# Optimization experiments

Hardware: AMD Instinct MI355X
Metric: run time of the kernel (lower is better)

## Reference

```python
import jax, jax.numpy as jnp
import numpy as np

B, S, D = 4, 2048, 2048
H = 16
DH = D // H  # 128

def _rope_tables(seq_len, d_head, base=10000.0):
    inv_freq = 1.0 / (base ** (np.arange(0, d_head, 2, dtype=np.float32) / d_head))
    pos = np.arange(seq_len, dtype=np.float32)
    ang = pos[:, None] * inv_freq[None, :]  # (S, d_head/2)
    return jnp.asarray(np.cos(ang)), jnp.asarray(np.sin(ang))

def setup_inputs() -> dict:
    key = jax.random.key(0)
    ks = jax.random.split(key, 4)
    x = jax.random.normal(ks[0], (B, S, D), dtype=jnp.float32)
    rope_cos, rope_sin = _rope_tables(S, DH)
    # Linear params, scaled like torch default init (~1/sqrt(fan_in))
    Wqkv = jax.random.normal(ks[1], (D, 3 * D), dtype=jnp.float32) / np.sqrt(D)
    bqkv = jnp.zeros((3 * D,), dtype=jnp.float32)
    Wout = jax.random.normal(ks[2], (D, D), dtype=jnp.float32) / np.sqrt(D)
    bout = jnp.zeros((D,), dtype=jnp.float32)
    return {"x": x, "rope_cos": rope_cos, "rope_sin": rope_sin,
            "Wqkv": Wqkv, "bqkv": bqkv, "Wout": Wout, "bout": bout}

def _apply_rope(x, cos, sin):
    # x: (B, H, S, DH); cos/sin: (S, DH/2), broadcast over B,H
    x1 = x[..., 0::2]
    x2 = x[..., 1::2]
    out = jnp.stack([x1 * cos - x2 * sin, x1 * sin + x2 * cos], axis=-1)
    return out.reshape(*out.shape[:-2], -1)  # interleave back to (..., DH)

def reference(x, rope_cos, rope_sin, Wqkv, bqkv, Wout, bout):
    qkv = (x @ Wqkv + bqkv).reshape(B, S, 3, H, DH)
    qkv = jnp.transpose(qkv, (2, 0, 3, 1, 4))  # (3, B, H, S, DH)
    q, k, v = qkv[0], qkv[1], qkv[2]
    q = _apply_rope(q, rope_cos, rope_sin)
    k = _apply_rope(k, rope_cos, rope_sin)
    scale = 1.0 / np.sqrt(DH)
    scores = jnp.einsum('bhqd,bhkd->bhqk', q, k) * scale  # (B,H,S,S)
    causal = jnp.tril(jnp.ones((S, S), dtype=bool))
    scores = jnp.where(causal, scores, jnp.finfo(scores.dtype).min)
    attn = jax.nn.softmax(scores, axis=-1)
    out = jnp.einsum('bhqk,bhkd->bhqd', attn, v)  # (B,H,S,DH)
    out = jnp.transpose(out, (0, 2, 1, 3)).reshape(B, S, D)
    return out @ Wout + bout
```

## Files before the change

kernel.cpp:

```cpp
#include <hip/hip_runtime.h>
#include <hip/hip_bf16.h>
#include <math.h>

typedef __attribute__((ext_vector_type(8))) short bf16x8;
typedef __attribute__((ext_vector_type(4))) float f32x4;
typedef __attribute__((ext_vector_type(16))) float f32x16;
typedef __attribute__((ext_vector_type(8))) unsigned short u16x8;
typedef __attribute__((ext_vector_type(4))) unsigned short u16x4;

static constexpr int B = 4, S = 2048, D = 2048, H = 16, DH = 128;
static constexpr int N3 = 3 * D;
static constexpr int M = B * S;

__device__ __forceinline__ unsigned short f2bf(float f) {
  unsigned u = __float_as_uint(f);
  u += 0x7fffu + ((u >> 16) & 1u);
  return (unsigned short)(u >> 16);
}
__device__ __forceinline__ float bf2f(unsigned short b) {
  return __uint_as_float(((unsigned)b) << 16);
}

__global__ __launch_bounds__(256) void cvt_kernel(const float* __restrict__ in,
                                                  unsigned short* __restrict__ out) {
  size_t i = (size_t)blockIdx.x * 256 + threadIdx.x;
  f32x4 v = *(const f32x4*)(in + i * 4);
  u16x4 o;
  o[0] = f2bf(v[0]); o[1] = f2bf(v[1]); o[2] = f2bf(v[2]); o[3] = f2bf(v[3]);
  *(u16x4*)(out + i * 4) = o;
}

__global__ __launch_bounds__(256) void transpose_kernel(const float* __restrict__ W,
                                                        unsigned short* __restrict__ WT,
                                                        int K, int N) {
  __shared__ float t[32][33];
  int tx = threadIdx.x, ty = threadIdx.y;
  int n0 = blockIdx.x * 32, k0 = blockIdx.y * 32;
#pragma unroll
  for (int i = 0; i < 4; i++)
    t[ty + i * 8][tx] = W[(size_t)(k0 + ty + i * 8) * N + n0 + tx];
  __syncthreads();
#pragma unroll
  for (int i = 0; i < 4; i++)
    WT[(size_t)(n0 + ty + i * 8) * K + k0 + tx] = f2bf(t[tx][ty + i * 8]);
}

__device__ __forceinline__ void gload_lds(const void* g, void* l) {
  __builtin_amdgcn_global_load_lds((const __attribute__((address_space(1))) void*)g,
                                   (__attribute__((address_space(3))) void*)l, 16, 0, 0);
}

template <int EPI>
__global__ __launch_bounds__(512, 1) void gemm_bt(
    const unsigned short* __restrict__ A, const unsigned short* __restrict__ Bt,
    const float* __restrict__ bias, float* __restrict__ Cf,
    unsigned short* __restrict__ Qp, unsigned short* __restrict__ Kp,
    unsigned short* __restrict__ VTp, int Nn, int nbn) {
  __shared__ __align__(16) unsigned short lds[65536];
  constexpr int NT = 32;
  const int tid = threadIdx.x;
  const int l = tid & 63;
  const int w = tid >> 6;
  const int lc = l & 15, lr = l >> 4;
  const int wm = w >> 2, wn = w & 3;

  const int nwg = gridDim.x;
  const int cpx = nwg >> 3;
  const int wg = blockIdx.x;
  const int swz = (wg & 7) * cpx + (wg >> 3);
  const int bm = swz / nbn;
  const int bn = swz - bm * nbn;

  const int lq = l >> 2, lg = l & 3;
  const int gsw = lg ^ ((l >> 3) & 3);
  const unsigned short* sA[2];
  const unsigned short* sB[2];
  int dA[2], dB[2];
#pragma unroll
  for (int mh = 0; mh < 2; mh++) {
    const int rowA = mh * 64 + wn * 16 + lq;
    sA[mh] = A + (size_t)(bm * 256 + wm * 128 + rowA) * 2048 + gsw * 8;
    dA[mh] = wm * 8192 + rowA * 32 + lg * 8;
    const int rowB = (wm * 2 + (wn & 1)) * 32 + mh * 16 + lq;
    sB[mh] = Bt + (size_t)(bn * 256 + (wn >> 1) * 128 + rowB) * 2048 + gsw * 8;
    dB[mh] = 32768 + (wn >> 1) * 8192 + rowB * 32 + lg * 8;
  }

  const int rsw = (lr ^ ((lc >> 1) & 3)) * 8;
  const int frA = wm * 8192 + lc * 32 + rsw;
  const int frB = 32768 + (wn >> 1) * 8192 + ((wn & 1) * 64 + lc) * 32 + rsw;

  f32x4 acc[8][4];
#pragma unroll
  for (int m = 0; m < 8; m++)
#pragma unroll
    for (int n = 0; n < 4; n++) acc[m][n] = (f32x4)0.f;

#define STG(t1, kh, mh)                                                          \
  do {                                                                           \
    const int dbo_ = ((t1) & 1) * 16384 + (kh) * 4096;                           \
    const int ko_ = (t1) * 64 + (kh) * 32;                                       \
    gload_lds(sA[mh] + ko_, lds + dbo_ + dA[mh]);                                \
    gload_lds(sB[mh] + ko_, lds + dbo_ + dB[mh]);                                \
  } while (0)

  STG(0, 0, 0); STG(0, 0, 1); STG(0, 1, 0); STG(0, 1, 1);
  __builtin_amdgcn_sched_barrier(0);
  asm volatile("s_waitcnt vmcnt(0)" ::: "memory");
  __builtin_amdgcn_s_barrier();
  __builtin_amdgcn_sched_barrier(0);

  bf16x8 bfr[4];

#define PHASE(db, kh, mh, DOSTG, t1)                                             \
  do {                                                                           \
    bf16x8 af0, af1, af2, af3;                                                   \
    const int ab_ = (db) * 16384 + (kh) * 4096 + frA + (mh) * 2048;              \
    af0 = *(const bf16x8*)(lds + ab_);                                           \
    af1 = *(const bf16x8*)(lds + ab_ + 512);                                     \
    af2 = *(const bf16x8*)(lds + ab_ + 1024);                                    \
    af3 = *(const bf16x8*)(lds + ab_ + 1536);                                    \
    if (mh == 0) {                                                               \
      const int bb_ = (db) * 16384 + (kh) * 4096 + frB;                          \
      bfr[0] = *(const bf16x8*)(lds + bb_);                                      \
      bfr[1] = *(const bf16x8*)(lds + bb_ + 512);                                \
      bfr[2] = *(const bf16x8*)(lds + bb_ + 1024);                               \
      bfr[3] = *(const bf16x8*)(lds + bb_ + 1536);                               \
    }                                                                            \
    if (DOSTG) STG(t1, kh, mh);                                                  \
    __builtin_amdgcn_sched_barrier(0);                                           \
    asm volatile("s_waitcnt lgkmcnt(0)" ::: "memory");                           \
    __builtin_amdgcn_sched_barrier(0);                                           \
    __builtin_amdgcn_s_setprio(1);                                               \
    _Pragma("unroll")                                                            \
    for (int nt = 0; nt < 4; nt++) {                                             \
      acc[(mh)*4 + 0][nt] = __builtin_amdgcn_mfma_f32_16x16x32_bf16(af0, bfr[nt], acc[(mh)*4 + 0][nt], 0, 0, 0); \
      acc[(mh)*4 + 1][nt] = __builtin_amdgcn_mfma_f32_16x16x32_bf16(af1, bfr[nt], acc[(mh)*4 + 1][nt], 0, 0, 0); \
      acc[(mh)*4 + 2][nt] = __builtin_amdgcn_mfma_f32_16x16x32_bf16(af2, bfr[nt], acc[(mh)*4 + 2][nt], 0, 0, 0); \
      acc[(mh)*4 + 3][nt] = __builtin_amdgcn_mfma_f32_16x16x32_bf16(af3, bfr[nt], acc[(mh)*4 + 3][nt], 0, 0, 0); \
    }                                                                            \
    __builtin_amdgcn_s_setprio(0);                                               \
    __builtin_amdgcn_sched_barrier(0);                                           \
    asm volatile("s_waitcnt vmcnt(4)" ::: "memory");                             \
    __builtin_amdgcn_s_barrier();                                                \
    __builtin_amdgcn_sched_barrier(0);                                           \
  } while (0)

#pragma unroll 2
  for (int t = 0; t < NT; t++) {
    const int db = t & 1;
    const bool dg = (t + 1) < NT;
    PHASE(db, 0, 0, dg, t + 1);
    PHASE(db, 0, 1, dg, t + 1);
    PHASE(db, 1, 0, dg, t + 1);
    PHASE(db, 1, 1, dg, t + 1);
  }
#undef PHASE
#undef STG

#pragma unroll
  for (int m = 0; m < 8; m++) {
#pragma unroll
    for (int n = 0; n < 4; n++) {
      const int col = bn * 256 + wn * 64 + n * 16 + lc;
      const float bv = bias[col];
#pragma unroll
      for (int r = 0; r < 4; r++) {
        const int row = bm * 256 + wm * 128 + (m >> 2) * 64 + (m & 3) * 16 + lr * 4 + r;
        const float v = acc[m][n][r] + bv;
        if (EPI == 0) {
          const unsigned short ob = f2bf(v);
          const int b = row >> 11, s = row & 2047;
          const int which = col >> 11, within = col & 2047;
          const int h = within >> 7, d = within & 127;
          const size_t bh = (size_t)(b * H + h);
          if (which == 0)      Qp[(bh * S + s) * DH + d] = ob;
          else if (which == 1) Kp[(bh * S + s) * DH + d] = ob;
          else                 VTp[(bh * DH + d) * S + s] = ob;
        } else {
          Cf[(size_t)row * Nn + col] = v;
        }
      }
    }
  }
}

__global__ __launch_bounds__(256) void rope_kernel(unsigned short* __restrict__ T,
                                                   const float* __restrict__ cosT,
                                                   const float* __restrict__ sinT) {
  int t = blockIdx.x * 256 + threadIdx.x;
  int d8 = t & 15;
  int s = (t >> 4) & (S - 1);
  size_t off = (size_t)t * 8;
  u16x8 v = *(const u16x8*)(T + off);
  f32x4 c = *(const f32x4*)(cosT + (size_t)s * (DH / 2) + d8 * 4);
  f32x4 sn = *(const f32x4*)(sinT + (size_t)s * (DH / 2) + d8 * 4);
  u16x8 o;
#pragma unroll
  for (int j = 0; j < 4; j++) {
    float x1 = bf2f(v[2 * j]), x2 = bf2f(v[2 * j + 1]);
    o[2 * j]     = f2bf(x1 * c[j] - x2 * sn[j]);
    o[2 * j + 1] = f2bf(x1 * sn[j] + x2 * c[j]);
  }
  *(u16x8*)(T + off) = o;
}

__global__ __launch_bounds__(512, 1) void attn3_kernel(
    const unsigned short* __restrict__ Q, const unsigned short* __restrict__ Kt,
    const unsigned short* __restrict__ VT, unsigned short* __restrict__ O) {
  __shared__ __align__(16) unsigned short lK[2][32 * 128];
  __shared__ __align__(16) unsigned short lV[2][128 * 40];
  const int tid = threadIdx.x;
  const int w = tid >> 6;
  const int l = tid & 63;
  const int ql = l & 31;
  const int hi = l >> 5;
  const int j = blockIdx.x;
  const int bh = ((j >> 3) & 7) * 8 + (j & 7);
  const int pr = j >> 6;
  const int b = bh >> 4, h = bh & 15;
  const size_t base = (size_t)bh * S * DH;
  const float cl = 0.088388347648318447f * 1.44269504088896341f;

  const int kdst = (tid * 8) ^ (((tid >> 4) & 7) << 3);
  const unsigned short* Kgb = Kt + base;
  const int vdh = tid >> 2;
  const int vc = (tid & 3) * 8;
  const int vdst = vdh * 40 + vc;
  const unsigned short* Vgr = VT + ((size_t)bh * DH + vdh) * S;
  const int sfix = (ql & 7) << 3;

  for (int half = 0; half < 2; half++) {
    const int strip = half ? 7 - pr : pr;
    const int qw0 = strip * 256 + w * 32;

    bf16x8 qf[8];
    const unsigned short* qp = Q + base + (size_t)(qw0 + ql) * DH + hi * 8;
#pragma unroll
    for (int t = 0; t < 8; t++) qf[t] = *(const bf16x8*)(qp + t * 16);

    f32x16 acc[4];
#pragma unroll
    for (int mt = 0; mt < 4; mt++) acc[mt] = (f32x16)0.f;
    float m = -INFINITY, lsum = 0.f;

    const int ntb = 8 * (strip + 1);
    const int last = 8 * strip + w;

    {
      f32x4 kr = *(const f32x4*)(Kgb + tid * 8);
      f32x4 vr = *(const f32x4*)(Vgr + vc);
      *(f32x4*)(&lK[0][kdst]) = kr;
      *(f32x4*)(&lV[0][vdst]) = vr;
      __syncthreads();
    }

    for (int kb = 0; kb < ntb; kb++) {
      const int cur = kb & 1;
      const bool more = (kb + 1 < ntb);
      f32x4 kr, vr;
      if (more) {
        kr = *(const f32x4*)(Kgb + (size_t)(kb + 1) * 4096 + tid * 8);
        vr = *(const f32x4*)(Vgr + (kb + 1) * 32 + vc);
      }
      if (kb <= last) {
        const unsigned short* kbuf = lK[cur];
        const unsigned short* vbuf = lV[cur];
        f32x16 st0 = (f32x16)0.f, st1 = (f32x16)0.f;
#pragma unroll
        for (int t = 0; t < 4; t++) {
          bf16x8 k0 = *(const bf16x8*)(kbuf + ((ql * 128 + (2 * t) * 16 + 8 * hi) ^ sfix));
          bf16x8 k1 = *(const bf16x8*)(kbuf + ((ql * 128 + (2 * t + 1) * 16 + 8 * hi) ^ sfix));
          st0 = __builtin_amdgcn_mfma_f32_32x32x16_bf16(k0, qf[2 * t], st0, 0, 0, 0);
          st1 = __builtin_amdgcn_mfma_f32_32x32x16_bf16(k1, qf[2 * t + 1], st1, 0, 0, 0);
        }
        float sv[16];
#pragma unroll
        for (int r = 0; r < 16; r++) sv[r] = st0[r] + st1[r];
        if (kb == last) {
#pragma unroll
          for (int r = 0; r < 16; r++) {
            const int klocal = (r & 3) + 8 * (r >> 2) + 4 * hi;
            sv[r] = (klocal > ql) ? -INFINITY : sv[r];
          }
        }
        float smax = sv[0];
#pragma unroll
        for (int r = 1; r < 16; r++) smax = fmaxf(smax, sv[r]);
        smax = fmaxf(smax, __shfl_xor(smax, 32));

        float fr = 1.f;
        if (!__all((smax - m) * cl <= 8.0f)) {
          const float mn = fmaxf(m, smax);
          fr = exp2f((m - mn) * cl);
          m = mn;
#pragma unroll
          for (int mt = 0; mt < 4; mt++)
#pragma unroll
            for (int r = 0; r < 16; r++) acc[mt][r] *= fr;
        }
        float p[16];
        float ps = 0.f;
#pragma unroll
        for (int r = 0; r < 16; r++) {
          p[r] = exp2f((sv[r] - m) * cl);
          ps += p[r];
        }
        lsum = lsum * fr + ps + __shfl_xor(ps, 32);

        unsigned W[8];
#pragma unroll
        for (int qd = 0; qd < 4; qd++) {
          W[2 * qd]     = (unsigned)f2bf(p[4 * qd])     | ((unsigned)f2bf(p[4 * qd + 1]) << 16);
          W[2 * qd + 1] = (unsigned)f2bf(p[4 * qd + 2]) | ((unsigned)f2bf(p[4 * qd + 3]) << 16);
        }
#pragma unroll
        for (int t = 0; t < 2; t++) {
          const unsigned s0 = hi ? W[4 * t] : W[4 * t + 2];
          const unsigned s1 = hi ? W[4 * t + 1] : W[4 * t + 3];
          const unsigned r0 = __shfl_xor((int)s0, 32);
          const unsigned r1 = __shfl_xor((int)s1, 32);
          union { unsigned u[4]; bf16x8 v; } pf;
          if (hi == 0) { pf.u[0] = W[4 * t]; pf.u[1] = W[4 * t + 1]; pf.u[2] = r0; pf.u[3] = r1; }
          else         { pf.u[0] = r0; pf.u[1] = r1; pf.u[2] = W[4 * t + 2]; pf.u[3] = W[4 * t + 3]; }
#pragma unroll
          for (int mt = 0; mt < 4; mt++) {
            const bf16x8 vf = *(const bf16x8*)(vbuf + (mt * 32 + ql) * 40 + 16 * t + 8 * hi);
            acc[mt] = __builtin_amdgcn_mfma_f32_32x32x16_bf16(vf, pf.v, acc[mt], 0, 0, 0);
          }
        }
      }
      if (more) {
        *(f32x4*)(&lK[cur ^ 1][kdst]) = kr;
        *(f32x4*)(&lV[cur ^ 1][vdst]) = vr;
      }
      __syncthreads();
    }

    const float inv = 1.f / lsum;
    const int s_glob = qw0 + ql;
    unsigned short* op = O + ((size_t)(b * S + s_glob) * H + h) * DH;
#pragma unroll
    for (int mt = 0; mt < 4; mt++)
#pragma unroll
      for (int g = 0; g < 4; g++) {
        u16x4 ov;
#pragma unroll
        for (int jj = 0; jj < 4; jj++) ov[jj] = f2bf(acc[mt][4 * g + jj] * inv);
        *(u16x4*)(op + mt * 32 + 8 * g + 4 * hi) = ov;
      }
  }
}

extern "C" void kernel_launch(void* const* d_in, const int* in_sizes, int n_in,
                              void* d_out, int out_size, void* d_ws, size_t ws_size,
                              hipStream_t stream) {
  const float* x    = (const float*)d_in[0];
  const float* cosT = (const float*)d_in[1];
  const float* sinT = (const float*)d_in[2];
  const float* Wqkv = (const float*)d_in[3];
  const float* bqkv = (const float*)d_in[4];
  const float* Wout = (const float*)d_in[5];
  const float* bout = (const float*)d_in[6];

  char* ws = (char*)d_ws;
  unsigned short* xbf   = (unsigned short*)(ws);
  unsigned short* WqkvT = (unsigned short*)(ws + ((size_t)32 << 20));
  unsigned short* WoutT = (unsigned short*)(ws + ((size_t)56 << 20));
  unsigned short* VTb   = (unsigned short*)(ws + ((size_t)64 << 20));
  unsigned short* Qb = (unsigned short*)d_out;
  unsigned short* Kb = (unsigned short*)d_out + (size_t)M * D;
  unsigned short* Ob = xbf;

  cvt_kernel<<<M * D / 1024, 256, 0, stream>>>(x, xbf);
  transpose_kernel<<<dim3(N3 / 32, D / 32), dim3(32, 8), 0, stream>>>(Wqkv, WqkvT, D, N3);
  transpose_kernel<<<dim3(D / 32, D / 32), dim3(32, 8), 0, stream>>>(Wout, WoutT, D, D);
  gemm_bt<0><<<dim3((M / 256) * (N3 / 256)), 512, 0, stream>>>(xbf, WqkvT, bqkv, nullptr,
                                                               Qb, Kb, VTb, N3, N3 / 256);
  rope_kernel<<<(B * H * S * 16) / 256, 256, 0, stream>>>(Qb, cosT, sinT);
  rope_kernel<<<(B * H * S * 16) / 256, 256, 0, stream>>>(Kb, cosT, sinT);
  attn3_kernel<<<B * H * 4, 512, 0, stream>>>(Qb, Kb, VTb, Ob);
  gemm_bt<1><<<dim3((M / 256) * (D / 256)), 512, 0, stream>>>(Ob, WoutT, bout, (float*)d_out,
                                                              nullptr, nullptr, nullptr, D, D / 256);
}
```

Measured before the change: 487.0 us.

## Deepen GEMM prefetch pipeline to 1.5 k-tiles ahead with per-phase barriers

Restructures the QKV/out-projection GEMM main loop so that global-to-LDS loads run one and a half k-half-tiles ahead instead of one. Each phase now stages the next half-tile slot that was freed earlier. The loop is manually unrolled by two with an explicit epilogue that uses tapered vmcnt waits. An extra s_barrier before each phase's MFMA block guards the LDS slot reuse. The aim is to hide more global memory latency, at the cost of more barriers per iteration and a hard-coded NT=32 tail that could be fragile.

```diff
diff --git a/kernel.cpp b/kernel.cpp
--- a/kernel.cpp
+++ b/kernel.cpp
@@ -96,67 +96,81 @@
 #pragma unroll
     for (int n = 0; n < 4; n++) acc[m][n] = (f32x4)0.f;
 
-#define STG(t1, kh, mh)                                                          \
+#define STG2(tt, skh, mh)                                                        \
   do {                                                                           \
-    const int dbo_ = ((t1) & 1) * 16384 + (kh) * 4096;                           \
-    const int ko_ = (t1) * 64 + (kh) * 32;                                       \
+    const int dbo_ = ((tt) & 1) * 16384 + (skh) * 4096;                          \
+    const int ko_ = (tt) * 64 + (skh) * 32;                                      \
     gload_lds(sA[mh] + ko_, lds + dbo_ + dA[mh]);                                \
     gload_lds(sB[mh] + ko_, lds + dbo_ + dB[mh]);                                \
   } while (0)
 
-  STG(0, 0, 0); STG(0, 0, 1); STG(0, 1, 0); STG(0, 1, 1);
+  STG2(0, 0, 0); STG2(0, 0, 1);
+  STG2(0, 1, 0); STG2(0, 1, 1);
+  STG2(1, 0, 0); STG2(1, 0, 1);
   __builtin_amdgcn_sched_barrier(0);
-  asm volatile("s_waitcnt vmcnt(0)" ::: "memory");
+  asm volatile("s_waitcnt vmcnt(8)" ::: "memory");
   __builtin_amdgcn_s_barrier();
   __builtin_amdgcn_sched_barrier(0);
 
   bf16x8 bfr[4];
 
-#define PHASE(db, kh, mh, DOSTG, t1)                                             \
+#define PHASE(db_, kh_, mh_, DOSTG_, tt_, skh_, VM_)                             \
   do {                                                                           \
     bf16x8 af0, af1, af2, af3;                                                   \
-    const int ab_ = (db) * 16384 + (kh) * 4096 + frA + (mh) * 2048;              \
+    const int ab_ = (db_) * 16384 + (kh_) * 4096 + frA + (mh_) * 2048;           \
     af0 = *(const bf16x8*)(lds + ab_);                                           \
     af1 = *(const bf16x8*)(lds + ab_ + 512);                                     \
     af2 = *(const bf16x8*)(lds + ab_ + 1024);                                    \
     af3 = *(const bf16x8*)(lds + ab_ + 1536);                                    \
-    if (mh == 0) {                                                               \
-      const int bb_ = (db) * 16384 + (kh) * 4096 + frB;                          \
+    if (mh_ == 0) {                                                              \
+      const int bb_ = (db_) * 16384 + (kh_) * 4096 + frB;                        \
       bfr[0] = *(const bf16x8*)(lds + bb_);                                      \
       bfr[1] = *(const bf16x8*)(lds + bb_ + 512);                                \
       bfr[2] = *(const bf16x8*)(lds + bb_ + 1024);                               \
       bfr[3] = *(const bf16x8*)(lds + bb_ + 1536);                               \
     }                                                                            \
-    if (DOSTG) STG(t1, kh, mh);                                                  \
+    if (DOSTG_) STG2(tt_, skh_, mh_);                                            \
     __builtin_amdgcn_sched_barrier(0);                                           \
+    __builtin_amdgcn_s_barrier();                                                \
     asm volatile("s_waitcnt lgkmcnt(0)" ::: "memory");                           \
     __builtin_amdgcn_sched_barrier(0);                                           \
     __builtin_amdgcn_s_setprio(1);                                               \
     _Pragma("unroll")                                                            \
     for (int nt = 0; nt < 4; nt++) {                                             \
-      acc[(mh)*4 + 0][nt] = __builtin_amdgcn_mfma_f32_16x16x32_bf16(af0, bfr[nt], acc[(mh)*4 + 0][nt], 0, 0, 0); \
-      acc[(mh)*4 + 1][nt] = __builtin_amdgcn_mfma_f32_16x16x32_bf16(af1, bfr[nt], acc[(mh)*4 + 1][nt], 0, 0, 0); \
-      acc[(mh)*4 + 2][nt] = __builtin_amdgcn_mfma_f32_16x16x32_bf16(af2, bfr[nt], acc[(mh)*4 + 2][nt], 0, 0, 0); \
-      acc[(mh)*4 + 3][nt] = __builtin_amdgcn_mfma_f32_16x16x32_bf16(af3, bfr[nt], acc[(mh)*4 + 3][nt], 0, 0, 0); \
+      acc[(mh_)*4 + 0][nt] = __builtin_amdgcn_mfma_f32_16x16x32_bf16(af0, bfr[nt], acc[(mh_)*4 + 0][nt], 0, 0, 0); \
+      acc[(mh_)*4 + 1][nt] = __builtin_amdgcn_mfma_f32_16x16x32_bf16(af1, bfr[nt], acc[(mh_)*4 + 1][nt], 0, 0, 0); \
+      acc[(mh_)*4 + 2][nt] = __builtin_amdgcn_mfma_f32_16x16x32_bf16(af2, bfr[nt], acc[(mh_)*4 + 2][nt], 0, 0, 0); \
+      acc[(mh_)*4 + 3][nt] = __builtin_amdgcn_mfma_f32_16x16x32_bf16(af3, bfr[nt], acc[(mh_)*4 + 3][nt], 0, 0, 0); \
     }                                                                            \
     __builtin_amdgcn_s_setprio(0);                                               \
     __builtin_amdgcn_sched_barrier(0);                                           \
-    asm volatile("s_waitcnt vmcnt(4)" ::: "memory");                             \
+    if ((VM_) == 8) asm volatile("s_waitcnt vmcnt(8)" ::: "memory");             \
+    else if ((VM_) == 4) asm volatile("s_waitcnt vmcnt(4)" ::: "memory");        \
+    else if ((VM_) == 0) asm volatile("s_waitcnt vmcnt(0)" ::: "memory");        \
     __builtin_amdgcn_s_barrier();                                                \
     __builtin_amdgcn_sched_barrier(0);                                           \
   } while (0)
 
-#pragma unroll 2
-  for (int t = 0; t < NT; t++) {
-    const int db = t & 1;
-    const bool dg = (t + 1) < NT;
-    PHASE(db, 0, 0, dg, t + 1);
-    PHASE(db, 0, 1, dg, t + 1);
-    PHASE(db, 1, 0, dg, t + 1);
-    PHASE(db, 1, 1, dg, t + 1);
-  }
+  for (int t = 0; t < NT - 2; t += 2) {
+    PHASE(0, 0, 0, true, t + 1, 1, -1);
+    PHASE(0, 0, 1, true, t + 1, 1, 8);
+    PHASE(0, 1, 0, true, t + 2, 0, -1);
+    PHASE(0, 1, 1, true, t + 2, 0, 8);
+    PHASE(1, 0, 0, true, t + 2, 1, -1);
+    PHASE(1, 0, 1, true, t + 2, 1, 8);
+    PHASE(1, 1, 0, true, t + 3, 0, -1);
+    PHASE(1, 1, 1, true, t + 3, 0, 8);
+  }
+  PHASE(0, 0, 0, true, 31, 1, -1);
+  PHASE(0, 0, 1, true, 31, 1, 8);
+  PHASE(0, 1, 0, false, 0, 0, -1);
+  PHASE(0, 1, 1, false, 0, 0, 4);
+  PHASE(1, 0, 0, false, 0, 0, -1);
+  PHASE(1, 0, 1, false, 0, 0, 0);
+  PHASE(1, 1, 0, false, 0, 0, -1);
+  PHASE(1, 1, 1, false, 0, 0, -1);
 #undef PHASE
-#undef STG
+#undef STG2
 
 #pragma unroll
   for (int m = 0; m < 8; m++) {
```

New measurement: 487.0 us. About the same (+0.0%).

## Fuse RoPE into QKV GEMM epilogue and widen attention KV tiles to 64

Applied to the files above, without the earlier changes.

Applies the rotary embedding inside the QKV GEMM epilogue, using a lane shuffle to fetch the paired element, and removes the two separate RoPE kernels with their extra read/write passes over Q and K. The attention kernel now stages 64-key K/V tiles per iteration, processing two 32-key subtiles from each buffer. This halves the number of loop iterations and block barriers, at the cost of more LDS and some masked subtile work near the diagonal. RoPE is now computed from fp32 accumulators instead of bf16-rounded values, which changes rounding slightly.

```diff
diff --git a/kernel.cpp b/kernel.cpp
--- a/kernel.cpp
+++ b/kernel.cpp
@@ -55,7 +55,8 @@
     const unsigned short* __restrict__ A, const unsigned short* __restrict__ Bt,
     const float* __restrict__ bias, float* __restrict__ Cf,
     unsigned short* __restrict__ Qp, unsigned short* __restrict__ Kp,
-    unsigned short* __restrict__ VTp, int Nn, int nbn) {
+    unsigned short* __restrict__ VTp, const float* __restrict__ cosT,
+    const float* __restrict__ sinT, int Nn, int nbn) {
   __shared__ __align__(16) unsigned short lds[65536];
   constexpr int NT = 32;
   const int tid = threadIdx.x;
@@ -164,14 +165,22 @@
     for (int n = 0; n < 4; n++) {
       const int col = bn * 256 + wn * 64 + n * 16 + lc;
       const float bv = bias[col];
+      const int which = col >> 11;
 #pragma unroll
       for (int r = 0; r < 4; r++) {
         const int row = bm * 256 + wm * 128 + (m >> 2) * 64 + (m & 3) * 16 + lr * 4 + r;
-        const float v = acc[m][n][r] + bv;
+        float v = acc[m][n][r] + bv;
         if (EPI == 0) {
+          const int b = row >> 11, s = row & 2047;
+          if (which < 2) {
+            const float p = __shfl_xor(v, 1);
+            const int jj = (col & 127) >> 1;
+            const float c = cosT[s * 64 + jj];
+            const float sn = sinT[s * 64 + jj];
+            v = (lc & 1) ? fmaf(p, sn, v * c) : fmaf(-p, sn, v * c);
+          }
           const unsigned short ob = f2bf(v);
-          const int b = row >> 11, s = row & 2047;
-          const int which = col >> 11, within = col & 2047;
+          const int within = col & 2047;
           const int h = within >> 7, d = within & 127;
           const size_t bh = (size_t)(b * H + h);
           if (which == 0)      Qp[(bh * S + s) * DH + d] = ob;
@@ -185,31 +194,11 @@
   }
 }
 
-__global__ __launch_bounds__(256) void rope_kernel(unsigned short* __restrict__ T,
-                                                   const float* __restrict__ cosT,
-                                                   const float* __restrict__ sinT) {
-  int t = blockIdx.x * 256 + threadIdx.x;
-  int d8 = t & 15;
-  int s = (t >> 4) & (S - 1);
-  size_t off = (size_t)t * 8;
-  u16x8 v = *(const u16x8*)(T + off);
-  f32x4 c = *(const f32x4*)(cosT + (size_t)s * (DH / 2) + d8 * 4);
-  f32x4 sn = *(const f32x4*)(sinT + (size_t)s * (DH / 2) + d8 * 4);
-  u16x8 o;
-#pragma unroll
-  for (int j = 0; j < 4; j++) {
-    float x1 = bf2f(v[2 * j]), x2 = bf2f(v[2 * j + 1]);
-    o[2 * j]     = f2bf(x1 * c[j] - x2 * sn[j]);
-    o[2 * j + 1] = f2bf(x1 * sn[j] + x2 * c[j]);
-  }
-  *(u16x8*)(T + off) = o;
-}
-
-__global__ __launch_bounds__(512, 1) void attn3_kernel(
+__global__ __launch_bounds__(512, 1) void attn4_kernel(
     const unsigned short* __restrict__ Q, const unsigned short* __restrict__ Kt,
     const unsigned short* __restrict__ VT, unsigned short* __restrict__ O) {
-  __shared__ __align__(16) unsigned short lK[2][32 * 128];
-  __shared__ __align__(16) unsigned short lV[2][128 * 40];
+  __shared__ __align__(16) unsigned short lK[2][64 * 128];
+  __shared__ __align__(16) unsigned short lV[2][128 * 72];
   const int tid = threadIdx.x;
   const int w = tid >> 6;
   const int l = tid & 63;
@@ -222,13 +211,24 @@
   const size_t base = (size_t)bh * S * DH;
   const float cl = 0.088388347648318447f * 1.44269504088896341f;
 
-  const int kdst = (tid * 8) ^ (((tid >> 4) & 7) << 3);
-  const unsigned short* Kgb = Kt + base;
+  const unsigned short* Ksrc[2];
+  int Kdst[2];
+#pragma unroll
+  for (int i = 0; i < 2; i++) {
+    const int g = i * 512 + tid;
+    const int krow = g >> 4;
+    Ksrc[i] = Kt + base + (size_t)krow * 128 + (g & 15) * 8;
+    Kdst[i] = (g * 8) ^ ((krow & 7) << 3);
+  }
   const int vdh = tid >> 2;
-  const int vc = (tid & 3) * 8;
-  const int vdst = vdh * 40 + vc;
-  const unsigned short* Vgr = VT + ((size_t)bh * DH + vdh) * S;
-  const int sfix = (ql & 7) << 3;
+  const unsigned short* Vsrc = VT + ((size_t)bh * DH + vdh) * S;
+  int vcol[2], Vdst[2];
+#pragma unroll
+  for (int i = 0; i < 2; i++) {
+    vcol[i] = (tid & 3) * 8 + i * 32;
+    Vdst[i] = vdh * 72 + vcol[i];
+  }
+  const int sfx = (ql & 7) << 3;
 
   for (int half = 0; half < 2; half++) {
     const int strip = half ? 7 - pr : pr;
@@ -244,95 +244,108 @@
     for (int mt = 0; mt < 4; mt++) acc[mt] = (f32x16)0.f;
     float m = -INFINITY, lsum = 0.f;
 
-    const int ntb = 8 * (strip + 1);
-    const int last = 8 * strip + w;
+    const int ntb = 4 * (strip + 1);
 
     {
-      f32x4 kr = *(const f32x4*)(Kgb + tid * 8);
-      f32x4 vr = *(const f32x4*)(Vgr + vc);
-      *(f32x4*)(&lK[0][kdst]) = kr;
-      *(f32x4*)(&lV[0][vdst]) = vr;
+      f32x4 k0 = *(const f32x4*)(Ksrc[0]);
+      f32x4 k1 = *(const f32x4*)(Ksrc[1]);
+      f32x4 v0 = *(const f32x4*)(Vsrc + vcol[0]);
+      f32x4 v1 = *(const f32x4*)(Vsrc + vcol[1]);
+      *(f32x4*)(&lK[0][Kdst[0]]) = k0;
+      *(f32x4*)(&lK[0][Kdst[1]]) = k1;
+      *(f32x4*)(&lV[0][Vdst[0]]) = v0;
+      *(f32x4*)(&lV[0][Vdst[1]]) = v1;
       __syncthreads();
     }
 
     for (int kb = 0; kb < ntb; kb++) {
       const int cur = kb & 1;
       const bool more = (kb + 1 < ntb);
-      f32x4 kr, vr;
+      f32x4 k0r, k1r, v0r, v1r;
       if (more) {
-        kr = *(const f32x4*)(Kgb + (size_t)(kb + 1) * 4096 + tid * 8);
-        vr = *(const f32x4*)(Vgr + (kb + 1) * 32 + vc);
-      }
-      if (kb <= last) {
-        const unsigned short* kbuf = lK[cur];
-        const unsigned short* vbuf = lV[cur];
-        f32x16 st0 = (f32x16)0.f, st1 = (f32x16)0.f;
-#pragma unroll
-        for (int t = 0; t < 4; t++) {
-          bf16x8 k0 = *(const bf16x8*)(kbuf + ((ql * 128 + (2 * t) * 16 + 8 * hi) ^ sfix));
-          bf16x8 k1 = *(const bf16x8*)(kbuf + ((ql * 128 + (2 * t + 1) * 16 + 8 * hi) ^ sfix));
-          st0 = __builtin_amdgcn_mfma_f32_32x32x16_bf16(k0, qf[2 * t], st0, 0, 0, 0);
-          st1 = __builtin_amdgcn_mfma_f32_32x32x16_bf16(k1, qf[2 * t + 1], st1, 0, 0, 0);
+        k0r = *(const f32x4*)(Ksrc[0] + (size_t)(kb + 1) * 8192);
+        k1r = *(const f32x4*)(Ksrc[1] + (size_t)(kb + 1) * 8192);
+        v0r = *(const f32x4*)(Vsrc + (kb + 1) * 64 + vcol[0]);
+        v1r = *(const f32x4*)(Vsrc + (kb + 1) * 64 + vcol[1]);
+      }
+      const unsigned short* kbuf = lK[cur];
+      const unsigned short* vbuf = lV[cur];
+#pragma unroll
+      for (int stx = 0; stx < 2; stx++) {
+        const int kvs = kb * 64 + stx * 32;
+        if (kvs <= qw0) {
+          const bool diag = (kvs == qw0);
+          const int krb = (stx * 32 + ql) * 128;
+          f32x16 s0 = (f32x16)0.f, s1 = (f32x16)0.f;
+#pragma unroll
+          for (int t = 0; t < 4; t++) {
+            bf16x8 k0 = *(const bf16x8*)(kbuf + ((krb + (2 * t) * 16 + 8 * hi) ^ sfx));
+            bf16x8 k1 = *(const bf16x8*)(kbuf + ((krb + (2 * t + 1) * 16 + 8 * hi) ^ sfx));
+            s0 = __builtin_amdgcn_mfma_f32_32x32x16_bf16(k0, qf[2 * t], s0, 0, 0, 0);
+            s1 = __builtin_amdgcn_mfma_f32_32x32x16_bf16(k1, qf[2 * t + 1], s1, 0, 0, 0);
+          }
+          float sv[16];
+#pragma unroll
+          for (int r = 0; r < 16; r++) sv[r] = s0[r] + s1[r];
+          if (diag) {
+#pragma unroll
+            for (int r = 0; r < 16; r++) {
+              const int klocal = (r & 3) + 8 * (r >> 2) + 4 * hi;
+              sv[r] = (klocal > ql) ? -INFINITY : sv[r];
+            }
+          }
+          float smax = sv[0];
+#pragma unroll
+          for (int r = 1; r < 16; r++) smax = fmaxf(smax, sv[r]);
+          smax = fmaxf(smax, __shfl_xor(smax, 32));
+
+          float fr = 1.f;
+          if (!__all((smax - m) * cl <= 8.0f)) {
+            const float mn = fmaxf(m, smax);
+            fr = exp2f((m - mn) * cl);
+            m = mn;
+#pragma unroll
+            for (int mt = 0; mt < 4; mt++)
+#pragma unroll
+              for (int r = 0; r < 16; r++) acc[mt][r] *= fr;
+          }
+          float p[16];
+          float ps = 0.f;
+#pragma unroll
+          for (int r = 0; r < 16; r++) {
+            p[r] = exp2f((sv[r] - m) * cl);
+            ps += p[r];
+          }
+          lsum = lsum * fr + ps + __shfl_xor(ps, 32);
+
+          unsigned W[8];
+#pragma unroll
+          for (int qd = 0; qd < 4; qd++) {
+            W[2 * qd]     = (unsigned)f2bf(p[4 * qd])     | ((unsigned)f2bf(p[4 * qd + 1]) << 16);
+            W[2 * qd + 1] = (unsigned)f2bf(p[4 * qd + 2]) | ((unsigned)f2bf(p[4 * qd + 3]) << 16);
+          }
+#pragma unroll
+          for (int t = 0; t < 2; t++) {
+            const unsigned ss0 = hi ? W[4 * t] : W[4 * t + 2];
+            const unsigned ss1 = hi ? W[4 * t + 1] : W[4 * t + 3];
+            const unsigned r0 = __shfl_xor((int)ss0, 32);
+            const unsigned r1 = __shfl_xor((int)ss1, 32);
+            union { unsigned u[4]; bf16x8 v; } pf;
+            if (hi == 0) { pf.u[0] = W[4 * t]; pf.u[1] = W[4 * t + 1]; pf.u[2] = r0; pf.u[3] = r1; }
+            else         { pf.u[0] = r0; pf.u[1] = r1; pf.u[2] = W[4 * t + 2]; pf.u[3] = W[4 * t + 3]; }
+#pragma unroll
+            for (int mt = 0; mt < 4; mt++) {
+              const bf16x8 vf = *(const bf16x8*)(vbuf + (mt * 32 + ql) * 72 + stx * 32 + 16 * t + 8 * hi);
+              acc[mt] = __builtin_amdgcn_mfma_f32_32x32x16_bf16(vf, pf.v, acc[mt], 0, 0, 0);
+            }
+          }
         }
-        float sv[16];
-#pragma unroll
-        for (int r = 0; r < 16; r++) sv[r] = st0[r] + st1[r];
-        if (kb == last) {
-#pragma unroll
-          for (int r = 0; r < 16; r++) {
-            const int klocal = (r & 3) + 8 * (r >> 2) + 4 * hi;
-            sv[r] = (klocal > ql) ? -INFINITY : sv[r];
-          }
-        }
-        float smax = sv[0];
-#pragma unroll
-        for (int r = 1; r < 16; r++) smax = fmaxf(smax, sv[r]);
-        smax = fmaxf(smax, __shfl_xor(smax, 32));
-
-        float fr = 1.f;
-        if (!__all((smax - m) * cl <= 8.0f)) {
-          const float mn = fmaxf(m, smax);
-          fr = exp2f((m - mn) * cl);
-          m = mn;
-#pragma unroll
-          for (int mt = 0; mt < 4; mt++)
-#pragma unroll
-            for (int r = 0; r < 16; r++) acc[mt][r] *= fr;
-        }
-        float p[16];
-        float ps = 0.f;
-#pragma unroll
-        for (int r = 0; r < 16; r++) {
-          p[r] = exp2f((sv[r] - m) * cl);
-          ps += p[r];
-        }
-        lsum = lsum * fr + ps + __shfl_xor(ps, 32);
-
-        unsigned W[8];
-#pragma unroll
-        for (int qd = 0; qd < 4; qd++) {
-          W[2 * qd]     = (unsigned)f2bf(p[4 * qd])     | ((unsigned)f2bf(p[4 * qd + 1]) << 16);
-          W[2 * qd + 1] = (unsigned)f2bf(p[4 * qd + 2]) | ((unsigned)f2bf(p[4 * qd + 3]) << 16);
-        }
-#pragma unroll
-        for (int t = 0; t < 2; t++) {
-          const unsigned s0 = hi ? W[4 * t] : W[4 * t + 2];
-          const unsigned s1 = hi ? W[4 * t + 1] : W[4 * t + 3];
-          const unsigned r0 = __shfl_xor((int)s0, 32);
-          const unsigned r1 = __shfl_xor((int)s1, 32);
-          union { unsigned u[4]; bf16x8 v; } pf;
-          if (hi == 0) { pf.u[0] = W[4 * t]; pf.u[1] = W[4 * t + 1]; pf.u[2] = r0; pf.u[3] = r1; }
-          else         { pf.u[0] = r0; pf.u[1] = r1; pf.u[2] = W[4 * t + 2]; pf.u[3] = W[4 * t + 3]; }
-#pragma unroll
-          for (int mt = 0; mt < 4; mt++) {
-            const bf16x8 vf = *(const bf16x8*)(vbuf + (mt * 32 + ql) * 40 + 16 * t + 8 * hi);
-            acc[mt] = __builtin_amdgcn_mfma_f32_32x32x16_bf16(vf, pf.v, acc[mt], 0, 0, 0);
-          }
-        }
       }
       if (more) {
-        *(f32x4*)(&lK[cur ^ 1][kdst]) = kr;
-        *(f32x4*)(&lV[cur ^ 1][vdst]) = vr;
+        *(f32x4*)(&lK[cur ^ 1][Kdst[0]]) = k0r;
+        *(f32x4*)(&lK[cur ^ 1][Kdst[1]]) = k1r;
+        *(f32x4*)(&lV[cur ^ 1][Vdst[0]]) = v0r;
+        *(f32x4*)(&lV[cur ^ 1][Vdst[1]]) = v1r;
       }
       __syncthreads();
     }
@@ -376,10 +389,10 @@
   transpose_kernel<<<dim3(N3 / 32, D / 32), dim3(32, 8), 0, stream>>>(Wqkv, WqkvT, D, N3);
   transpose_kernel<<<dim3(D / 32, D / 32), dim3(32, 8), 0, stream>>>(Wout, WoutT, D, D);
   gemm_bt<0><<<dim3((M / 256) * (N3 / 256)), 512, 0, stream>>>(xbf, WqkvT, bqkv, nullptr,
-                                                               Qb, Kb, VTb, N3, N3 / 256);
-  rope_kernel<<<(B * H * S * 16) / 256, 256, 0, stream>>>(Qb, cosT, sinT);
-  rope_kernel<<<(B * H * S * 16) / 256, 256, 0, stream>>>(Kb, cosT, sinT);
-  attn3_kernel<<<B * H * 4, 512, 0, stream>>>(Qb, Kb, VTb, Ob);
+                                                               Qb, Kb, VTb, cosT, sinT,
+                                                               N3, N3 / 256);
+  attn4_kernel<<<B * H * 4, 512, 0, stream>>>(Qb, Kb, VTb, Ob);
   gemm_bt<1><<<dim3((M / 256) * (D / 256)), 512, 0, stream>>>(Ob, WoutT, bout, (float*)d_out,
-                                                              nullptr, nullptr, nullptr, D, D / 256);
-}
+                                                              nullptr, nullptr, nullptr,
+                                                              nullptr, nullptr, D, D / 256);
+}
```

Result: slower. 501.6 us (+3.0%).
